# Performance work log

Measured on AMD Instinct MI355X. Metric: run time of the kernel, lower is better.

Reference implementation:

```python
import jax, jax.numpy as jnp
import numpy as np

CUTOFF = 0.05

def _freq_filter(x_chw, filter_type):
    # x_chw: [C,H,W] = batch element 0, detached in the original (stop_gradient)
    x = jax.lax.stop_gradient(x_chw)
    C, H, W = x.shape
    a = jnp.abs(x)
    mn = a.min(axis=(1, 2), keepdims=True)
    ptp = a.max(axis=(1, 2), keepdims=True) - mn
    # np.uint8(255*(a-mn)/ptp): values in [0,255], cast truncates -> floor
    q = jnp.floor(255.0 * (a - mn) / ptp)
    f = jnp.fft.fftshift(jnp.fft.fft2(q), axes=(-2, -1))
    crow, ccol = H // 2, W // 2
    dr, dc = int(CUTOFF * crow), int(CUTOFF * ccol)
    m = jnp.zeros((H, W), dtype=q.dtype)
    m = m.at[crow - dr:crow + dr, ccol - dc:ccol + dc].set(1.0)
    if filter_type == 'low_pass':
        m = 1.0 - m  # note: original 'low_pass' actually removes low freqs
    out = jnp.abs(jnp.fft.ifft2(jnp.fft.ifftshift(f * m, axes=(-2, -1))))
    return out.astype(x_chw.dtype)  # [C,H,W]

def _conv1x1(x, w, b):
    # x: [B,C,H,W], w: [O,C], b: [O]
    return jnp.einsum('oc,bchw->bohw', w, x) + b[None, :, None, None]

def setup_inputs() -> dict:
    key = jax.random.key(0)
    ks = jax.random.split(key, 7)
    B, C, H, W = 1, 256, 96, 96
    fuse = jax.random.normal(ks[0], (B, C, H, W), dtype=jnp.float32)
    s = 1.0 / np.sqrt(C)
    Wq = jax.random.normal(ks[1], (C, C), dtype=jnp.float32) * s
    bq = jax.random.normal(ks[2], (C,), dtype=jnp.float32) * 0.01
    Wk = jax.random.normal(ks[3], (C, C), dtype=jnp.float32) * s
    bk = jax.random.normal(ks[4], (C,), dtype=jnp.float32) * 0.01
    Wv = jax.random.normal(ks[5], (C, C), dtype=jnp.float32) * s
    bv = jax.random.normal(ks[6], (C,), dtype=jnp.float32) * 0.01
    return {"fuse": fuse, "Wq": Wq, "bq": bq, "Wk": Wk, "bk": bk, "Wv": Wv, "bv": bv}

def reference(fuse, Wq, bq, Wk, bk, Wv, bv):
    B, C, H, W = fuse.shape
    scale = 1.0 / (C ** 0.5)
    # frequency-filtered maps (computed from batch 0, broadcast to all batches)
    FQ = jnp.broadcast_to(_freq_filter(fuse[0], 'high_pass'), fuse.shape)
    FK = jnp.broadcast_to(_freq_filter(fuse[0], 'low_pass'), fuse.shape)
    fuse_Query = _conv1x1(FQ, Wq, bq).reshape(B, C, H * W)     # [B,C,HW]
    fuse_Q_mask = fuse_Query.reshape(B * H, C * W)             # [B*H, C*W]
    fuse_Query_t = jnp.transpose(fuse_Query, (0, 2, 1))        # [B,HW,C]
    fuse_Key = _conv1x1(FK, Wk, bk).reshape(B, C, H * W)       # [B,C,HW]
    Fuse_Q_mask = jnp.max(fuse_Q_mask, axis=0, keepdims=True)  # [1, C*W]
    mask_KQ = jnp.einsum('bnc,bcm->bnm', fuse_Query_t, fuse_Key) * scale  # [B,HW,HW]
    mask_KQ = jax.nn.softmax(mask_KQ, axis=0)  # softmax over batch dim (as in original)
    mask_KQ = jnp.max(mask_KQ, axis=1)                         # [B,HW]
    mask_KQ = mask_KQ.reshape(-1, W)                           # [B*H, W]
    mask_KQ = jnp.max(mask_KQ, axis=-1, keepdims=True)         # [B*H, 1]
    mask = (mask_KQ @ Fuse_Q_mask).reshape(B, C, H, W)
    fuse_Value = _conv1x1(fuse, Wv, bv)
    return fuse_Value + fuse_Value * mask
```

## Files before the change

kernel.cpp:

```cpp
#include <hip/hip_runtime.h>
#include <math.h>

#define CCH 256
#define HW  9216
#define CW  24576
#define TWO_PI 6.28318530717958647692f

typedef __attribute__((ext_vector_type(8))) short short8;
typedef __attribute__((ext_vector_type(4))) float f32x4;

__device__ inline unsigned short f2bf(float f) {
    unsigned u = __float_as_uint(f);
    unsigned r = (u + 0x7FFFu + ((u >> 16) & 1u)) >> 16;
    return (unsigned short)r;
}

__global__ __launch_bounds__(768) void k_pre(const float* __restrict__ x,
                                             const float* __restrict__ Wq,
                                             const float* __restrict__ Wv,
                                             short8* __restrict__ Wqt,
                                             short8* __restrict__ Wvt,
                                             unsigned* __restrict__ FQm,
                                             float* __restrict__ Fg) {
    __shared__ float qa[HW];
    __shared__ float cs[96][2];
    __shared__ float Gp[8][96][5];
    __shared__ float Gs[96][6];
    __shared__ float red[24];
    __shared__ float s_mn, s_ptp;
    int bid = blockIdx.x, t = threadIdx.x;

    if (bid >= 256) {
        int widx = bid - 256;
        if (t < 256) {
            const float* src = (widx >= 32) ? Wv : Wq;
            short8* dst = (widx >= 32) ? Wvt : Wqt;
            int cidx = (widx & 31) * 256 + t;
            int ot = cidx >> 11, kc = (cidx >> 6) & 31, m = cidx & 63;
            const float* s = src + (ot * 64 + m) * 256 + kc * 8;
            short8 v;
            #pragma unroll
            for (int e = 0; e < 8; ++e) v[e] = (short)f2bf(s[e]);
            dst[cidx] = v;
        }
        return;
    }

    int c = bid;
    if (t < 96) FQm[c * 96 + t] = 0u;
    const float* xp = x + c * HW;
    if (t < 96) { float a = TWO_PI * (float)t / 96.0f; cs[t][0] = cosf(a); cs[t][1] = sinf(a); }
    float lo = 1e30f, hi = 0.f;
    #pragma unroll
    for (int i = 0; i < 12; ++i) {
        float a = fabsf(xp[t + i * 768]);
        qa[t + i * 768] = a;
        lo = fminf(lo, a);
        hi = fmaxf(hi, a);
    }
    #pragma unroll
    for (int d = 32; d; d >>= 1) {
        lo = fminf(lo, __shfl_xor(lo, d, 64));
        hi = fmaxf(hi, __shfl_xor(hi, d, 64));
    }
    if ((t & 63) == 0) { red[t >> 6] = lo; red[12 + (t >> 6)] = hi; }
    __syncthreads();
    if (t == 0) {
        lo = red[0]; hi = red[12];
        #pragma unroll
        for (int i = 1; i < 12; ++i) { lo = fminf(lo, red[i]); hi = fmaxf(hi, red[12 + i]); }
        s_mn = lo; s_ptp = hi - lo;
    }
    __syncthreads();
    float mn = s_mn, ptp = s_ptp;

    {
        int xx = t % 96, h = t / 96;
        float g0r = 0, g0i = 0, g1r = 0, g1i = 0, g2 = 0;
        for (int y = h * 12; y < h * 12 + 12; ++y) {
            float q = floorf(255.0f * (qa[y * 96 + xx] - mn) / ptp);
            float c1 = cs[y][0], s1 = cs[y][1];
            float c2 = c1 * c1 - s1 * s1, s2 = 2.0f * c1 * s1;
            g0r += q * c2; g0i += q * s2;
            g1r += q * c1; g1i += q * s1;
            g2  += q;
        }
        Gp[h][xx][0] = g0r; Gp[h][xx][1] = g0i;
        Gp[h][xx][2] = g1r; Gp[h][xx][3] = g1i;
        Gp[h][xx][4] = g2;
    }
    __syncthreads();
    if (t < 96) {
        #pragma unroll
        for (int j = 0; j < 5; ++j) {
            float s = 0.f;
            #pragma unroll
            for (int h = 0; h < 8; ++h) s += Gp[h][t][j];
            Gs[t][j] = s;
        }
        Gs[t][5] = 0.f;
    }
    __syncthreads();
    if (t < 64) {
        int coef = t >> 2, qq = t & 3;
        int ky = coef >> 2, kx = coef & 3;
        float fr = 0, fi = 0;
        for (int xx = qq * 24; xx < qq * 24 + 24; ++xx) {
            float c1 = cs[xx][0], s1 = cs[xx][1];
            float er, ei;
            if (kx == 0)      { er = c1 * c1 - s1 * s1; ei = 2.0f * c1 * s1; }
            else if (kx == 1) { er = c1; ei = s1; }
            else if (kx == 2) { er = 1.f; ei = 0.f; }
            else              { er = c1; ei = -s1; }
            float gr, gi;
            if (ky == 0)      { gr = Gs[xx][0]; gi = Gs[xx][1]; }
            else if (ky == 1) { gr = Gs[xx][2]; gi = Gs[xx][3]; }
            else if (ky == 2) { gr = Gs[xx][4]; gi = 0.f; }
            else              { gr = Gs[xx][2]; gi = -Gs[xx][3]; }
            fr += gr * er - gi * ei;
            fi += gr * ei + gi * er;
        }
        fr += __shfl_xor(fr, 1, 64); fr += __shfl_xor(fr, 2, 64);
        fi += __shfl_xor(fi, 1, 64); fi += __shfl_xor(fi, 2, 64);
        if (qq == 0) {
            Fg[c * 32 + 2 * coef]     = fr;
            Fg[c * 32 + 2 * coef + 1] = fi;
        }
    }
}

__global__ __launch_bounds__(256) void k_gemmQ(const short8* __restrict__ Wqt,
                                               const float* __restrict__ Fg,
                                               const float* __restrict__ bq,
                                               unsigned* __restrict__ FQm) {
    __shared__ short8 As[2048];
    __shared__ short8 Bs[2048];
    __shared__ float Rs[2048][2];
    float (*fq)[64] = (float (*)[64])Rs;
    int tid = threadIdx.x;
    int pt_ = blockIdx.x;
    int p0 = pt_ * 64;

    int l = tid & 63, w = tid >> 6;
    int wr = w >> 1, wc = w & 1;
    int l15 = l & 15, quad = l >> 4;
    int abase = wr * 32 + l15;
    int bbase = wc * 32 + l15;

    short8 areg[8];
    #pragma unroll
    for (int i = 0; i < 8; ++i) areg[i] = Wqt[i * 256 + tid];

    int y0 = p0 / 96;
    {
        int yi = (tid >> 2) & 1, kx = tid & 3, cb = tid >> 3;
        float ay = TWO_PI * (float)(y0 + yi) / 96.0f;
        float cyv = cosf(ay), syv = sinf(ay);
        float cy2 = cyv * cyv - syv * syv, sy2 = 2.f * cyv * syv;
        float Ur[4] = { cy2, cyv, 1.f, cyv };
        float Ui[4] = { -sy2, -syv, 0.f, syv };
        #pragma unroll
        for (int i = 0; i < 8; ++i) {
            int cc = cb + i * 32;
            float rr = 0.f, ri = 0.f;
            #pragma unroll
            for (int ky = 0; ky < 4; ++ky) {
                float fr = Fg[cc * 32 + 2 * (ky * 4 + kx)];
                float fi = Fg[cc * 32 + 2 * (ky * 4 + kx) + 1];
                rr += fr * Ur[ky] - fi * Ui[ky];
                ri += fr * Ui[ky] + fi * Ur[ky];
            }
            Rs[cc * 8 + yi * 4 + kx][0] = rr;
            Rs[cc * 8 + yi * 4 + kx][1] = ri;
        }
    }
    __syncthreads();
    const float inv = 1.0f / 9216.0f;
    #pragma unroll
    for (int i = 0; i < 8; ++i) {
        int si = i * 256 + tid;
        int kcg = si >> 6, n = si & 63;
        int p = p0 + n;
        int y = p / 96, xx = p - y * 96;
        int yi = y - y0;
        float axv = TWO_PI * (float)xx / 96.0f;
        float cxv = cosf(axv), sxv = sinf(axv);
        float cx2 = cxv * cxv - sxv * sxv, sx2 = 2.f * cxv * sxv;
        float Tr[4] = { cx2, cxv, 1.f, cxv };
        float Ti[4] = { -sx2, -sxv, 0.f, sxv };
        short8 vv;
        #pragma unroll
        for (int e = 0; e < 8; ++e) {
            int rb = (kcg * 8 + e) * 8 + yi * 4;
            float ar = 0.f, ai = 0.f;
            #pragma unroll
            for (int kx = 0; kx < 4; ++kx) {
                float rr = Rs[rb + kx][0], ri = Rs[rb + kx][1];
                ar += rr * Tr[kx] - ri * Ti[kx];
                ai += rr * Ti[kx] + ri * Tr[kx];
            }
            vv[e] = (short)f2bf(sqrtf(ar * ar + ai * ai) * inv);
        }
        Bs[si] = vv;
    }
    __syncthreads();

    float vmax[2][4];
    #pragma unroll
    for (int ni = 0; ni < 2; ++ni)
        #pragma unroll
        for (int r = 0; r < 4; ++r) vmax[ni][r] = -3.0e38f;

    #pragma unroll
    for (int ot = 0; ot < 4; ++ot) {
        #pragma unroll
        for (int i = 0; i < 8; ++i) As[i * 256 + tid] = areg[i];
        __syncthreads();
        if (ot < 3) {
            #pragma unroll
            for (int i = 0; i < 8; ++i) areg[i] = Wqt[(ot + 1) * 2048 + i * 256 + tid];
        }
        f32x4 acc[2][2] = {};
        #pragma unroll
        for (int s = 0; s < 8; ++s) {
            int kc = s * 4 + quad;
            short8 a0 = As[kc * 64 + abase];
            short8 a1 = As[kc * 64 + abase + 16];
            short8 b0 = Bs[kc * 64 + bbase];
            short8 b1 = Bs[kc * 64 + bbase + 16];
            acc[0][0] = __builtin_amdgcn_mfma_f32_16x16x32_bf16(a0, b0, acc[0][0], 0, 0, 0);
            acc[0][1] = __builtin_amdgcn_mfma_f32_16x16x32_bf16(a0, b1, acc[0][1], 0, 0, 0);
            acc[1][0] = __builtin_amdgcn_mfma_f32_16x16x32_bf16(a1, b0, acc[1][0], 0, 0, 0);
            acc[1][1] = __builtin_amdgcn_mfma_f32_16x16x32_bf16(a1, b1, acc[1][1], 0, 0, 0);
        }
        #pragma unroll
        for (int ni = 0; ni < 2; ++ni) {
            #pragma unroll
            for (int r = 0; r < 4; ++r) {
                int o_lo = ot * 64 + wr * 32 + quad * 4 + r;
                float v = fmaxf(acc[0][ni][r] + bq[o_lo], acc[1][ni][r] + bq[o_lo + 16]);
                vmax[ni][r] = fmaxf(vmax[ni][r], v);
            }
        }
        __syncthreads();
    }

    #pragma unroll
    for (int ni = 0; ni < 2; ++ni)
        #pragma unroll
        for (int r = 0; r < 4; ++r)
            vmax[ni][r] = fmaxf(vmax[ni][r], __shfl_xor(vmax[ni][r], 32, 64));
    if (wr == 0 && quad < 2) {
        #pragma unroll
        for (int ni = 0; ni < 2; ++ni)
            #pragma unroll
            for (int r = 0; r < 4; ++r)
                fq[quad * 4 + r][wc * 32 + ni * 16 + l15] = vmax[ni][r];
    }
    __syncthreads();
    if (wr == 1 && quad < 2) {
        #pragma unroll
        for (int ni = 0; ni < 2; ++ni) {
            #pragma unroll
            for (int r = 0; r < 4; ++r) {
                int row = quad * 4 + r;
                int col = wc * 32 + ni * 16 + l15;
                float v = fmaxf(vmax[ni][r], fq[row][col]);
                int p = p0 + col;
                int k = row * HW + p;
                if (k >= CW) k -= CW;
                if (k >= CW) k -= CW;
                unsigned u = __float_as_uint(v);
                unsigned key = (u & 0x80000000u) ? ~u : (u | 0x80000000u);
                atomicMax(&FQm[k], key);
            }
        }
    }
}

__device__ inline float mdecode(unsigned key) {
    unsigned ub = (key & 0x80000000u) ? (key ^ 0x80000000u) : ~key;
    return __uint_as_float(ub);
}
__global__ __launch_bounds__(256) void k_gemmV(const short8* __restrict__ Wvt,
                                               const float* __restrict__ bv,
                                               const float* __restrict__ x,
                                               const unsigned* __restrict__ FQm,
                                               float* __restrict__ out) {
    __shared__ short8 As[2048];
    __shared__ short8 Bs[2048];
    int tid = threadIdx.x;
    int pt_ = blockIdx.x;
    int yv = blockIdx.y;
    int p0 = pt_ * 64;

    int l = tid & 63, w = tid >> 6;
    int wr = w >> 1, wc = w & 1;
    int l15 = l & 15, quad = l >> 4;
    int abase = wr * 32 + l15;
    int bbase = wc * 32 + l15;

    short8 areg[8];
    #pragma unroll
    for (int i = 0; i < 8; ++i) areg[i] = Wvt[(yv * 2) * 2048 + i * 256 + tid];

    #pragma unroll
    for (int i = 0; i < 8; ++i) {
        int si = i * 256 + tid;
        int KC = si >> 6, n = si & 63;
        const float* xb = x + (size_t)(KC * 8) * HW + p0 + n;
        short8 v;
        #pragma unroll
        for (int e = 0; e < 8; ++e) v[e] = (short)f2bf(xb[(size_t)e * HW]);
        Bs[si] = v;
    }

    float msk[2][4];
    #pragma unroll
    for (int ni = 0; ni < 2; ++ni) {
        #pragma unroll
        for (int r = 0; r < 4; ++r) {
            int row = (quad * 4 + r) & 7;
            int p = p0 + wc * 32 + ni * 16 + l15;
            int k = row * HW + p;
            if (k >= CW) k -= CW;
            if (k >= CW) k -= CW;
            msk[ni][r] = mdecode(FQm[k]);
        }
    }

    #pragma unroll
    for (int j = 0; j < 2; ++j) {
        int ot = yv * 2 + j;
        #pragma unroll
        for (int i = 0; i < 8; ++i) As[i * 256 + tid] = areg[i];
        __syncthreads();
        if (j == 0) {
            #pragma unroll
            for (int i = 0; i < 8; ++i) areg[i] = Wvt[(yv * 2 + 1) * 2048 + i * 256 + tid];
        }
        f32x4 acc[2][2] = {};
        #pragma unroll
        for (int s = 0; s < 8; ++s) {
            int kc = s * 4 + quad;
            short8 a0 = As[kc * 64 + abase];
            short8 a1 = As[kc * 64 + abase + 16];
            short8 b0 = Bs[kc * 64 + bbase];
            short8 b1 = Bs[kc * 64 + bbase + 16];
            acc[0][0] = __builtin_amdgcn_mfma_f32_16x16x32_bf16(a0, b0, acc[0][0], 0, 0, 0);
            acc[0][1] = __builtin_amdgcn_mfma_f32_16x16x32_bf16(a0, b1, acc[0][1], 0, 0, 0);
            acc[1][0] = __builtin_amdgcn_mfma_f32_16x16x32_bf16(a1, b0, acc[1][0], 0, 0, 0);
            acc[1][1] = __builtin_amdgcn_mfma_f32_16x16x32_bf16(a1, b1, acc[1][1], 0, 0, 0);
        }
        #pragma unroll
        for (int mi = 0; mi < 2; ++mi) {
            #pragma unroll
            for (int ni = 0; ni < 2; ++ni) {
                #pragma unroll
                for (int r = 0; r < 4; ++r) {
                    int o = ot * 64 + wr * 32 + mi * 16 + quad * 4 + r;
                    int p = p0 + wc * 32 + ni * 16 + l15;
                    out[(size_t)o * HW + p] = (acc[mi][ni][r] + bv[o]) * (1.0f + msk[ni][r]);
                }
            }
        }
        __syncthreads();
    }
}

extern "C" void kernel_launch(void* const* d_in, const int* in_sizes, int n_in,
                              void* d_out, int out_size, void* d_ws, size_t ws_size,
                              hipStream_t stream) {
    const float* fuse = (const float*)d_in[0];
    const float* Wq   = (const float*)d_in[1];
    const float* bq   = (const float*)d_in[2];
    const float* Wv   = (const float*)d_in[5];
    const float* bv   = (const float*)d_in[6];
    float* out = (float*)d_out;

    char* ws = (char*)d_ws;
    unsigned* FQm = (unsigned*)(ws);
    float*    Fg  = (float*)(ws + 98304);
    short8*   Wqt = (short8*)(ws + 131072);
    short8*   Wvt = (short8*)(ws + 262144);

    k_pre<<<320, 768, 0, stream>>>(fuse, Wq, Wv, Wqt, Wvt, FQm, Fg);
    k_gemmQ<<<144, 256, 0, stream>>>(Wqt, Fg, bq, FQm);
    k_gemmV<<<dim3(144, 2), 256, 0, stream>>>(Wvt, bv, fuse, FQm, out);
}
```

Before: 102.5 us.

## Merge Q and V GEMM kernels with spin-wait flag to overlap V GEMM with Q mask

Fuses the Q-mask GEMM kernel and the V GEMM kernel into one launch. Blocks with y=0 compute the Q mask and bump a global counter, while y=1,2 blocks compute their V GEMM results up front and spin on the counter before applying the mask in the epilogue. This removes one launch and lets the V GEMM overlap the Q work. It also precomputes per-column x twiddles into shared memory instead of recomputing sin/cos per element. The risk is deadlock or stall if Q blocks are not scheduled before the spinning V blocks, though 432 blocks likely all fit co-resident.

Result: slower. 112.1 us (+9.3%).

```diff
diff --git a/kernel.cpp b/kernel.cpp
--- a/kernel.cpp
+++ b/kernel.cpp
@@ -5,6 +5,7 @@
 #define HW  9216
 #define CW  24576
 #define TWO_PI 6.28318530717958647692f
+#define NQBLK 144u
 
 typedef __attribute__((ext_vector_type(8))) short short8;
 typedef __attribute__((ext_vector_type(4))) float f32x4;
@@ -21,7 +22,8 @@
                                              short8* __restrict__ Wqt,
                                              short8* __restrict__ Wvt,
                                              unsigned* __restrict__ FQm,
-                                             float* __restrict__ Fg) {
+                                             float* __restrict__ Fg,
+                                             unsigned* __restrict__ qdone) {
     __shared__ float qa[HW];
     __shared__ float cs[96][2];
     __shared__ float Gp[8][96][5];
@@ -48,6 +50,7 @@
 
     int c = bid;
     if (t < 96) FQm[c * 96 + t] = 0u;
+    if (bid == 0 && t == 96) *qdone = 0u;
     const float* xp = x + c * HW;
     if (t < 96) { float a = TWO_PI * (float)t / 96.0f; cs[t][0] = cosf(a); cs[t][1] = sinf(a); }
     float lo = 1e30f, hi = 0.f;
@@ -129,14 +132,24 @@
     }
 }
 
-__global__ __launch_bounds__(256) void k_gemmQ(const short8* __restrict__ Wqt,
-                                               const float* __restrict__ Fg,
-                                               const float* __restrict__ bq,
-                                               unsigned* __restrict__ FQm) {
+__device__ inline float mdecode(unsigned key) {
+    unsigned ub = (key & 0x80000000u) ? (key ^ 0x80000000u) : ~key;
+    return __uint_as_float(ub);
+}
+__global__ __launch_bounds__(256) void k_gemmQV(const short8* __restrict__ Wqt,
+                                                const short8* __restrict__ Wvt,
+                                                const float* __restrict__ Fg,
+                                                const float* __restrict__ bq,
+                                                const float* __restrict__ bv,
+                                                const float* __restrict__ x,
+                                                unsigned* __restrict__ FQm,
+                                                float* __restrict__ out,
+                                                unsigned* __restrict__ qdone) {
     __shared__ short8 As[2048];
     __shared__ short8 Bs[2048];
     __shared__ float Rs[2048][2];
     float (*fq)[64] = (float (*)[64])Rs;
+    float (*Ts)[9]  = (float (*)[9])As;
     int tid = threadIdx.x;
     int pt_ = blockIdx.x;
     int p0 = pt_ * 64;
@@ -147,159 +160,151 @@
     int abase = wr * 32 + l15;
     int bbase = wc * 32 + l15;
 
-    short8 areg[8];
-    #pragma unroll
-    for (int i = 0; i < 8; ++i) areg[i] = Wqt[i * 256 + tid];
-
-    int y0 = p0 / 96;
-    {
-        int yi = (tid >> 2) & 1, kx = tid & 3, cb = tid >> 3;
-        float ay = TWO_PI * (float)(y0 + yi) / 96.0f;
-        float cyv = cosf(ay), syv = sinf(ay);
-        float cy2 = cyv * cyv - syv * syv, sy2 = 2.f * cyv * syv;
-        float Ur[4] = { cy2, cyv, 1.f, cyv };
-        float Ui[4] = { -sy2, -syv, 0.f, syv };
+    if (blockIdx.y == 0) {
+        short8 areg[8];
+        #pragma unroll
+        for (int i = 0; i < 8; ++i) areg[i] = Wqt[i * 256 + tid];
+
+        int y0 = p0 / 96;
+        if (tid < 64) {
+            int xx = (p0 + tid) % 96;
+            float axv = TWO_PI * (float)xx / 96.0f;
+            float cxv = cosf(axv), sxv = sinf(axv);
+            float cx2 = cxv * cxv - sxv * sxv, sx2 = 2.f * cxv * sxv;
+            Ts[tid][0] = cx2;  Ts[tid][1] = cxv;  Ts[tid][2] = 1.f; Ts[tid][3] = cxv;
+            Ts[tid][4] = -sx2; Ts[tid][5] = -sxv; Ts[tid][6] = 0.f; Ts[tid][7] = sxv;
+        }
+        {
+            int yi = (tid >> 2) & 1, kx = tid & 3, cb = tid >> 3;
+            float ay = TWO_PI * (float)(y0 + yi) / 96.0f;
+            float cyv = cosf(ay), syv = sinf(ay);
+            float cy2 = cyv * cyv - syv * syv, sy2 = 2.f * cyv * syv;
+            float Ur[4] = { cy2, cyv, 1.f, cyv };
+            float Ui[4] = { -sy2, -syv, 0.f, syv };
+            #pragma unroll
+            for (int i = 0; i < 8; ++i) {
+                int cc = cb + i * 32;
+                float rr = 0.f, ri = 0.f;
+                #pragma unroll
+                for (int ky = 0; ky < 4; ++ky) {
+                    float fr = Fg[cc * 32 + 2 * (ky * 4 + kx)];
+                    float fi = Fg[cc * 32 + 2 * (ky * 4 + kx) + 1];
+                    rr += fr * Ur[ky] - fi * Ui[ky];
+                    ri += fr * Ui[ky] + fi * Ur[ky];
+                }
+                Rs[cc * 8 + yi * 4 + kx][0] = rr;
+                Rs[cc * 8 + yi * 4 + kx][1] = ri;
+            }
+        }
+        __syncthreads();
+        const float inv = 1.0f / 9216.0f;
         #pragma unroll
         for (int i = 0; i < 8; ++i) {
-            int cc = cb + i * 32;
-            float rr = 0.f, ri = 0.f;
-            #pragma unroll
-            for (int ky = 0; ky < 4; ++ky) {
-                float fr = Fg[cc * 32 + 2 * (ky * 4 + kx)];
-                float fi = Fg[cc * 32 + 2 * (ky * 4 + kx) + 1];
-                rr += fr * Ur[ky] - fi * Ui[ky];
-                ri += fr * Ui[ky] + fi * Ur[ky];
-            }
-            Rs[cc * 8 + yi * 4 + kx][0] = rr;
-            Rs[cc * 8 + yi * 4 + kx][1] = ri;
-        }
-    }
-    __syncthreads();
-    const float inv = 1.0f / 9216.0f;
-    #pragma unroll
-    for (int i = 0; i < 8; ++i) {
-        int si = i * 256 + tid;
-        int kcg = si >> 6, n = si & 63;
-        int p = p0 + n;
-        int y = p / 96, xx = p - y * 96;
-        int yi = y - y0;
-        float axv = TWO_PI * (float)xx / 96.0f;
-        float cxv = cosf(axv), sxv = sinf(axv);
-        float cx2 = cxv * cxv - sxv * sxv, sx2 = 2.f * cxv * sxv;
-        float Tr[4] = { cx2, cxv, 1.f, cxv };
-        float Ti[4] = { -sx2, -sxv, 0.f, sxv };
-        short8 vv;
-        #pragma unroll
-        for (int e = 0; e < 8; ++e) {
-            int rb = (kcg * 8 + e) * 8 + yi * 4;
-            float ar = 0.f, ai = 0.f;
-            #pragma unroll
-            for (int kx = 0; kx < 4; ++kx) {
-                float rr = Rs[rb + kx][0], ri = Rs[rb + kx][1];
-                ar += rr * Tr[kx] - ri * Ti[kx];
-                ai += rr * Ti[kx] + ri * Tr[kx];
-            }
-            vv[e] = (short)f2bf(sqrtf(ar * ar + ai * ai) * inv);
-        }
-        Bs[si] = vv;
-    }
-    __syncthreads();
-
-    float vmax[2][4];
-    #pragma unroll
-    for (int ni = 0; ni < 2; ++ni)
-        #pragma unroll
-        for (int r = 0; r < 4; ++r) vmax[ni][r] = -3.0e38f;
-
-    #pragma unroll
-    for (int ot = 0; ot < 4; ++ot) {
-        #pragma unroll
-        for (int i = 0; i < 8; ++i) As[i * 256 + tid] = areg[i];
+            int si = i * 256 + tid;
+            int kcg = si >> 6, n = si & 63;
+            int p = p0 + n;
+            int y = p / 96;
+            int yi = y - y0;
+            float Tr[4], Ti[4];
+            #pragma unroll
+            for (int j = 0; j < 4; ++j) { Tr[j] = Ts[n][j]; Ti[j] = Ts[n][4 + j]; }
+            short8 vv;
+            #pragma unroll
+            for (int e = 0; e < 8; ++e) {
+                int rb = (kcg * 8 + e) * 8 + yi * 4;
+                float ar = 0.f, ai = 0.f;
+                #pragma unroll
+                for (int kx = 0; kx < 4; ++kx) {
+                    float rr = Rs[rb + kx][0], ri = Rs[rb + kx][1];
+                    ar += rr * Tr[kx] - ri * Ti[kx];
+                    ai += rr * Ti[kx] + ri * Tr[kx];
+                }
+                vv[e] = (short)f2bf(sqrtf(ar * ar + ai * ai) * inv);
+            }
+            Bs[si] = vv;
+        }
         __syncthreads();
-        if (ot < 3) {
-            #pragma unroll
-            for (int i = 0; i < 8; ++i) areg[i] = Wqt[(ot + 1) * 2048 + i * 256 + tid];
-        }
-        f32x4 acc[2][2] = {};
-        #pragma unroll
-        for (int s = 0; s < 8; ++s) {
-            int kc = s * 4 + quad;
-            short8 a0 = As[kc * 64 + abase];
-            short8 a1 = As[kc * 64 + abase + 16];
-            short8 b0 = Bs[kc * 64 + bbase];
-            short8 b1 = Bs[kc * 64 + bbase + 16];
-            acc[0][0] = __builtin_amdgcn_mfma_f32_16x16x32_bf16(a0, b0, acc[0][0], 0, 0, 0);
-            acc[0][1] = __builtin_amdgcn_mfma_f32_16x16x32_bf16(a0, b1, acc[0][1], 0, 0, 0);
-            acc[1][0] = __builtin_amdgcn_mfma_f32_16x16x32_bf16(a1, b0, acc[1][0], 0, 0, 0);
-            acc[1][1] = __builtin_amdgcn_mfma_f32_16x16x32_bf16(a1, b1, acc[1][1], 0, 0, 0);
-        }
-        #pragma unroll
-        for (int ni = 0; ni < 2; ++ni) {
-            #pragma unroll
-            for (int r = 0; r < 4; ++r) {
-                int o_lo = ot * 64 + wr * 32 + quad * 4 + r;
-                float v = fmaxf(acc[0][ni][r] + bq[o_lo], acc[1][ni][r] + bq[o_lo + 16]);
-                vmax[ni][r] = fmaxf(vmax[ni][r], v);
-            }
+
+        float vmax[2][4];
+        #pragma unroll
+        for (int ni = 0; ni < 2; ++ni)
+            #pragma unroll
+            for (int r = 0; r < 4; ++r) vmax[ni][r] = -3.0e38f;
+
+        #pragma unroll
+        for (int ot = 0; ot < 4; ++ot) {
+            #pragma unroll
+            for (int i = 0; i < 8; ++i) As[i * 256 + tid] = areg[i];
+            __syncthreads();
+            if (ot < 3) {
+                #pragma unroll
+                for (int i = 0; i < 8; ++i) areg[i] = Wqt[(ot + 1) * 2048 + i * 256 + tid];
+            }
+            f32x4 acc[2][2] = {};
+            #pragma unroll
+            for (int s = 0; s < 8; ++s) {
+                int kc = s * 4 + quad;
+                short8 a0 = As[kc * 64 + abase];
+                short8 a1 = As[kc * 64 + abase + 16];
+                short8 b0 = Bs[kc * 64 + bbase];
+                short8 b1 = Bs[kc * 64 + bbase + 16];
+                acc[0][0] = __builtin_amdgcn_mfma_f32_16x16x32_bf16(a0, b0, acc[0][0], 0, 0, 0);
+                acc[0][1] = __builtin_amdgcn_mfma_f32_16x16x32_bf16(a0, b1, acc[0][1], 0, 0, 0);
+                acc[1][0] = __builtin_amdgcn_mfma_f32_16x16x32_bf16(a1, b0, acc[1][0], 0, 0, 0);
+                acc[1][1] = __builtin_amdgcn_mfma_f32_16x16x32_bf16(a1, b1, acc[1][1], 0, 0, 0);
+            }
+            #pragma unroll
+            for (int ni = 0; ni < 2; ++ni) {
+                #pragma unroll
+                for (int r = 0; r < 4; ++r) {
+                    int o_lo = ot * 64 + wr * 32 + quad * 4 + r;
+                    float v = fmaxf(acc[0][ni][r] + bq[o_lo], acc[1][ni][r] + bq[o_lo + 16]);
+                    vmax[ni][r] = fmaxf(vmax[ni][r], v);
+                }
+            }
+            __syncthreads();
+        }
+
+        #pragma unroll
+        for (int ni = 0; ni < 2; ++ni)
+            #pragma unroll
+            for (int r = 0; r < 4; ++r)
+                vmax[ni][r] = fmaxf(vmax[ni][r], __shfl_xor(vmax[ni][r], 32, 64));
+        if (wr == 0 && quad < 2) {
+            #pragma unroll
+            for (int ni = 0; ni < 2; ++ni)
+                #pragma unroll
+                for (int r = 0; r < 4; ++r)
+                    fq[quad * 4 + r][wc * 32 + ni * 16 + l15] = vmax[ni][r];
         }
         __syncthreads();
-    }
-
-    #pragma unroll
-    for (int ni = 0; ni < 2; ++ni)
-        #pragma unroll
-        for (int r = 0; r < 4; ++r)
-            vmax[ni][r] = fmaxf(vmax[ni][r], __shfl_xor(vmax[ni][r], 32, 64));
-    if (wr == 0 && quad < 2) {
-        #pragma unroll
-        for (int ni = 0; ni < 2; ++ni)
-            #pragma unroll
-            for (int r = 0; r < 4; ++r)
-                fq[quad * 4 + r][wc * 32 + ni * 16 + l15] = vmax[ni][r];
-    }
-    __syncthreads();
-    if (wr == 1 && quad < 2) {
-        #pragma unroll
-        for (int ni = 0; ni < 2; ++ni) {
-            #pragma unroll
-            for (int r = 0; r < 4; ++r) {
-                int row = quad * 4 + r;
-                int col = wc * 32 + ni * 16 + l15;
-                float v = fmaxf(vmax[ni][r], fq[row][col]);
-                int p = p0 + col;
-                int k = row * HW + p;
-                if (k >= CW) k -= CW;
-                if (k >= CW) k -= CW;
-                unsigned u = __float_as_uint(v);
-                unsigned key = (u & 0x80000000u) ? ~u : (u | 0x80000000u);
-                atomicMax(&FQm[k], key);
-            }
-        }
-    }
-}
-
-__device__ inline float mdecode(unsigned key) {
-    unsigned ub = (key & 0x80000000u) ? (key ^ 0x80000000u) : ~key;
-    return __uint_as_float(ub);
-}
-__global__ __launch_bounds__(256) void k_gemmV(const short8* __restrict__ Wvt,
-                                               const float* __restrict__ bv,
-                                               const float* __restrict__ x,
-                                               const unsigned* __restrict__ FQm,
-                                               float* __restrict__ out) {
-    __shared__ short8 As[2048];
-    __shared__ short8 Bs[2048];
-    int tid = threadIdx.x;
-    int pt_ = blockIdx.x;
-    int yv = blockIdx.y;
-    int p0 = pt_ * 64;
-
-    int l = tid & 63, w = tid >> 6;
-    int wr = w >> 1, wc = w & 1;
-    int l15 = l & 15, quad = l >> 4;
-    int abase = wr * 32 + l15;
-    int bbase = wc * 32 + l15;
-
+        if (wr == 1 && quad < 2) {
+            #pragma unroll
+            for (int ni = 0; ni < 2; ++ni) {
+                #pragma unroll
+                for (int r = 0; r < 4; ++r) {
+                    int row = quad * 4 + r;
+                    int col = wc * 32 + ni * 16 + l15;
+                    float v = fmaxf(vmax[ni][r], fq[row][col]);
+                    int p = p0 + col;
+                    int k = row * HW + p;
+                    if (k >= CW) k -= CW;
+                    if (k >= CW) k -= CW;
+                    unsigned u = __float_as_uint(v);
+                    unsigned key = (u & 0x80000000u) ? ~u : (u | 0x80000000u);
+                    atomicMax(&FQm[k], key);
+                }
+            }
+        }
+        __syncthreads();
+        if (tid == 0) {
+            __threadfence();
+            atomicAdd(qdone, 1u);
+        }
+        return;
+    }
+
+    int yv = blockIdx.y - 1;
     short8 areg[8];
     #pragma unroll
     for (int i = 0; i < 8; ++i) areg[i] = Wvt[(yv * 2) * 2048 + i * 256 + tid];
@@ -314,6 +319,48 @@
         for (int e = 0; e < 8; ++e) v[e] = (short)f2bf(xb[(size_t)e * HW]);
         Bs[si] = v;
     }
+    #pragma unroll
+    for (int i = 0; i < 8; ++i) As[i * 256 + tid] = areg[i];
+    __syncthreads();
+    #pragma unroll
+    for (int i = 0; i < 8; ++i) areg[i] = Wvt[(yv * 2 + 1) * 2048 + i * 256 + tid];
+
+    f32x4 accA[2][2] = {}, accB[2][2] = {};
+    #pragma unroll
+    for (int s = 0; s < 8; ++s) {
+        int kc = s * 4 + quad;
+        short8 a0 = As[kc * 64 + abase];
+        short8 a1 = As[kc * 64 + abase + 16];
+        short8 b0 = Bs[kc * 64 + bbase];
+        short8 b1 = Bs[kc * 64 + bbase + 16];
+        accA[0][0] = __builtin_amdgcn_mfma_f32_16x16x32_bf16(a0, b0, accA[0][0], 0, 0, 0);
+        accA[0][1] = __builtin_amdgcn_mfma_f32_16x16x32_bf16(a0, b1, accA[0][1], 0, 0, 0);
+        accA[1][0] = __builtin_amdgcn_mfma_f32_16x16x32_bf16(a1, b0, accA[1][0], 0, 0, 0);
+        accA[1][1] = __builtin_amdgcn_mfma_f32_16x16x32_bf16(a1, b1, accA[1][1], 0, 0, 0);
+    }
+    __syncthreads();
+    #pragma unroll
+    for (int i = 0; i < 8; ++i) As[i * 256 + tid] = areg[i];
+    __syncthreads();
+    #pragma unroll
+    for (int s = 0; s < 8; ++s) {
+        int kc = s * 4 + quad;
+        short8 a0 = As[kc * 64 + abase];
+        short8 a1 = As[kc * 64 + abase + 16];
+        short8 b0 = Bs[kc * 64 + bbase];
+        short8 b1 = Bs[kc * 64 + bbase + 16];
+        accB[0][0] = __builtin_amdgcn_mfma_f32_16x16x32_bf16(a0, b0, accB[0][0], 0, 0, 0);
+        accB[0][1] = __builtin_amdgcn_mfma_f32_16x16x32_bf16(a0, b1, accB[0][1], 0, 0, 0);
+        accB[1][0] = __builtin_amdgcn_mfma_f32_16x16x32_bf16(a1, b0, accB[1][0], 0, 0, 0);
+        accB[1][1] = __builtin_amdgcn_mfma_f32_16x16x32_bf16(a1, b1, accB[1][1], 0, 0, 0);
+    }
+
+    if (tid == 0) {
+        while (__hip_atomic_load(qdone, __ATOMIC_RELAXED, __HIP_MEMORY_SCOPE_AGENT) < NQBLK)
+            __builtin_amdgcn_s_sleep(8);
+        __threadfence();
+    }
+    __syncthreads();
 
     float msk[2][4];
     #pragma unroll
@@ -333,26 +380,6 @@
     for (int j = 0; j < 2; ++j) {
         int ot = yv * 2 + j;
         #pragma unroll
-        for (int i = 0; i < 8; ++i) As[i * 256 + tid] = areg[i];
-        __syncthreads();
-        if (j == 0) {
-            #pragma unroll
-            for (int i = 0; i < 8; ++i) areg[i] = Wvt[(yv * 2 + 1) * 2048 + i * 256 + tid];
-        }
-        f32x4 acc[2][2] = {};
-        #pragma unroll
-        for (int s = 0; s < 8; ++s) {
-            int kc = s * 4 + quad;
-            short8 a0 = As[kc * 64 + abase];
-            short8 a1 = As[kc * 64 + abase + 16];
-            short8 b0 = Bs[kc * 64 + bbase];
-            short8 b1 = Bs[kc * 64 + bbase + 16];
-            acc[0][0] = __builtin_amdgcn_mfma_f32_16x16x32_bf16(a0, b0, acc[0][0], 0, 0, 0);
-            acc[0][1] = __builtin_amdgcn_mfma_f32_16x16x32_bf16(a0, b1, acc[0][1], 0, 0, 0);
-            acc[1][0] = __builtin_amdgcn_mfma_f32_16x16x32_bf16(a1, b0, acc[1][0], 0, 0, 0);
-            acc[1][1] = __builtin_amdgcn_mfma_f32_16x16x32_bf16(a1, b1, acc[1][1], 0, 0, 0);
-        }
-        #pragma unroll
         for (int mi = 0; mi < 2; ++mi) {
             #pragma unroll
             for (int ni = 0; ni < 2; ++ni) {
@@ -360,11 +387,11 @@
                 for (int r = 0; r < 4; ++r) {
                     int o = ot * 64 + wr * 32 + mi * 16 + quad * 4 + r;
                     int p = p0 + wc * 32 + ni * 16 + l15;
-                    out[(size_t)o * HW + p] = (acc[mi][ni][r] + bv[o]) * (1.0f + msk[ni][r]);
+                    float a = j ? accB[mi][ni][r] : accA[mi][ni][r];
+                    out[(size_t)o * HW + p] = (a + bv[o]) * (1.0f + msk[ni][r]);
                 }
             }
         }
-        __syncthreads();
     }
 }
 
@@ -379,12 +406,12 @@
     float* out = (float*)d_out;
 
     char* ws = (char*)d_ws;
-    unsigned* FQm = (unsigned*)(ws);
-    float*    Fg  = (float*)(ws + 98304);
-    short8*   Wqt = (short8*)(ws + 131072);
-    short8*   Wvt = (short8*)(ws + 262144);
-
-    k_pre<<<320, 768, 0, stream>>>(fuse, Wq, Wv, Wqt, Wvt, FQm, Fg);
-    k_gemmQ<<<144, 256, 0, stream>>>(Wqt, Fg, bq, FQm);
-    k_gemmV<<<dim3(144, 2), 256, 0, stream>>>(Wvt, bv, fuse, FQm, out);
+    unsigned* FQm   = (unsigned*)(ws);
+    float*    Fg    = (float*)(ws + 98304);
+    short8*   Wqt   = (short8*)(ws + 131072);
+    short8*   Wvt   = (short8*)(ws + 262144);
+    unsigned* qdone = (unsigned*)(ws + 393216);
+
+    k_pre<<<320, 768, 0, stream>>>(fuse, Wq, Wv, Wqt, Wvt, FQm, Fg, qdone);
+    k_gemmQV<<<dim3(144, 3), 256, 0, stream>>>(Wqt, Wvt, Fg, bq, bv, fuse, FQm, out, qdone);
 }
```
